# Kernel optimization log

Measured on AMD Instinct MI355X. Metric: run time of the kernel, lower is better.

The kernel has to match this reference:

```python
import math
import jax, jax.numpy as jnp
import numpy as np

N_HEADS = 8
EMB = 512
BATCH = 256
NKEYS = 2048
NEG_INF = -jnp.inf


def setup_inputs() -> dict:
    key = jax.random.key(0)
    kq, kk, kv, kw, km = jax.random.split(key, 5)
    query = jax.random.normal(kq, (BATCH, 1, EMB), dtype=jnp.float32)
    keys = jax.random.normal(kk, (BATCH, NKEYS, EMB), dtype=jnp.float32)
    value = jax.random.normal(kv, (BATCH, NKEYS, EMB), dtype=jnp.float32)
    W_o = jax.random.normal(kw, (EMB, EMB), dtype=jnp.float32) / math.sqrt(EMB)
    mask = jax.random.randint(km, (BATCH, 1, NKEYS), 0, 2) == 1  # bool [B,1,K]
    return {"query": query, "key": keys, "value": value, "W_o": W_o, "mask": mask}


def _make_heads(v):
    # [B, N, D] -> [H, B, N, D/H]
    b, n, d = v.shape
    return v.reshape(b, n, N_HEADS, d // N_HEADS).transpose(2, 0, 1, 3)


def reference(query, key, value, W_o, mask):
    qh = _make_heads(query)            # [H, B, 1, dh]
    kh = _make_heads(key)              # [H, B, K, dh]
    vh = _make_heads(value)            # [H, B, K, dh]
    dh = qh.shape[-1]
    # scaled dot-product scores: [H, B, 1, K]
    u = jnp.einsum("hbqd,hbkd->hbqk", qh, kh) / math.sqrt(dh)
    # boolean masking: mask [B,1,K] broadcasts over heads
    logits = jnp.where(mask[None], NEG_INF, u)
    a = jax.nn.softmax(logits, axis=-1)            # [H, B, 1, K]
    oh = jnp.einsum("hbqk,hbkd->hbqd", a, vh)      # [H, B, 1, dh]
    # unmake heads: [H,B,1,dh] -> [B,1,H*dh]
    b = oh.shape[1]
    merged = oh.transpose(1, 2, 0, 3).reshape(b, 1, N_HEADS * dh)
    out = merged @ W_o.T                           # Linear, no bias
    return out
```

## Files before the change

### kernel.cpp

```cpp
#include <hip/hip_runtime.h>


#define NB    256
#define NK    2048
#define EMBD  512
#define NH    8
#define DH    64
#define CHUNKS 8
#define CKEYS  256
#define PREC   520
#define ACP    520

__device__ __forceinline__ void barrier_lgkm() {
    asm volatile("s_waitcnt lgkmcnt(0)" ::: "memory");
    __builtin_amdgcn_s_barrier();
}

__device__ __forceinline__ float4 ld4(const float* p) {
    return *reinterpret_cast<const float4*>(p);
}

__global__ __launch_bounds__(256) void attn_chunk_kernel(
    const float* __restrict__ q,
    const float* __restrict__ kptr,
    const float* __restrict__ vptr,
    const int* __restrict__ mask,
    float* __restrict__ partials)
{
    const int bid  = blockIdx.x;
    const int b    = bid >> 3;
    const int c    = bid & 7;
    const int t    = threadIdx.x;
    const int w    = t >> 6;
    const int lane = t & 63;
    const int hq   = lane >> 3;
    const int sub  = lane & 7;

    __shared__ int   klist[CKEYS];
    __shared__ int   wavecnt[4];
    __shared__ float redl[4][NH];
    __shared__ float accb[4 * ACP];

    const float* qb = q + (size_t)b * EMBD + lane * 8;
    const float4 qa = ld4(qb);
    const float4 qc = ld4(qb + 4);
    const float* kb = kptr + (size_t)b * NK * EMBD + lane * 8;
    const float* vb = vptr + (size_t)b * NK * EMBD + lane * 8;
    const int*   mrow = mask + (size_t)b * NK + c * CKEYS;

    const int myk = w * 64 + lane;
    const int mk  = mrow[myk];
    const unsigned long long bal = __ballot(mk == 0);
    if (lane == 0) wavecnt[w] = __popcll(bal);
    __syncthreads();
    int off = 0, nun = 0;
    #pragma unroll
    for (int i = 0; i < 4; ++i) {
        const int cc = wavecnt[i];
        off += (i < w) ? cc : 0;
        nun += cc;
    }
    const unsigned long long below = (1ull << lane) - 1ull;
    if (!mk) klist[off + __popcll(bal & below)] = c * CKEYS + myk;
    __syncthreads();

    float lsum = 0.f;
    float4 a0 = {0.f, 0.f, 0.f, 0.f};
    float4 a1 = {0.f, 0.f, 0.f, 0.f};
    {
        int key0 = (w < nun) ? klist[w] : -1;
        int key1 = (w + 4 < nun) ? klist[w + 4] : -1;
        float4 ka = {0,0,0,0}, kc = {0,0,0,0};
        float4 va = {0,0,0,0}, vc = {0,0,0,0};
        if (key0 >= 0) {
            const float* kk = kb + (size_t)key0 * EMBD;
            const float* vv = vb + (size_t)key0 * EMBD;
            ka = ld4(kk); kc = ld4(kk + 4);
            va = ld4(vv); vc = ld4(vv + 4);
        }
        for (int slot = w; slot < nun; slot += 4) {
            float4 nka = {0,0,0,0}, nkc = {0,0,0,0};
            float4 nva = {0,0,0,0}, nvc = {0,0,0,0};
            if (key1 >= 0) {
                const float* kk = kb + (size_t)key1 * EMBD;
                const float* vv = vb + (size_t)key1 * EMBD;
                nka = ld4(kk); nkc = ld4(kk + 4);
                nva = ld4(vv); nvc = ld4(vv + 4);
            }
            const int key2 = (slot + 8 < nun) ? klist[slot + 8] : -1;
            float sv = qa.x * ka.x + qa.y * ka.y + qa.z * ka.z + qa.w * ka.w
                     + qc.x * kc.x + qc.y * kc.y + qc.z * kc.z + qc.w * kc.w;
            sv += __shfl_xor(sv, 1, 8);
            sv += __shfl_xor(sv, 2, 8);
            sv += __shfl_xor(sv, 4, 8);
            const float p = __expf(sv * 0.125f);
            lsum += p;
            a0.x = fmaf(p, va.x, a0.x); a0.y = fmaf(p, va.y, a0.y);
            a0.z = fmaf(p, va.z, a0.z); a0.w = fmaf(p, va.w, a0.w);
            a1.x = fmaf(p, vc.x, a1.x); a1.y = fmaf(p, vc.y, a1.y);
            a1.z = fmaf(p, vc.z, a1.z); a1.w = fmaf(p, vc.w, a1.w);
            key0 = key1; ka = nka; kc = nkc; va = nva; vc = nvc; key1 = key2;
        }
    }
    if (sub == 0) redl[w][hq] = lsum;
    *reinterpret_cast<float4*>(&accb[w * ACP + lane * 8])     = a0;
    *reinterpret_cast<float4*>(&accb[w * ACP + lane * 8 + 4]) = a1;
    __syncthreads();

    float* rec = partials + (size_t)bid * PREC;
    if (t < NH)
        rec[t] = redl[0][t] + redl[1][t] + redl[2][t] + redl[3][t];
    const float s0 = accb[t] + accb[ACP + t] + accb[2 * ACP + t] + accb[3 * ACP + t];
    const int t2 = t + 256;
    const float s1 = accb[t2] + accb[ACP + t2] + accb[2 * ACP + t2] + accb[3 * ACP + t2];
    rec[8 + t]  = s0;
    rec[8 + t2] = s1;
}

__global__ __launch_bounds__(256) void merge_proj_kernel(
    const float* __restrict__ partials,
    const float* __restrict__ Wo,
    float* __restrict__ out)
{
    const int bt = blockIdx.x >> 3;
    const int jt = blockIdx.x & 7;
    const int t  = threadIdx.x;
    __shared__ float mrow[8][EMBD];
    __shared__ float sden[64];

    if (t < 64) {
        const int bb = t >> 3, h = t & 7;
        const float* base = partials + (size_t)((bt * 8 + bb) * 8) * PREC;
        float d = 0.f;
        #pragma unroll
        for (int cc = 0; cc < 8; ++cc) d += base[cc * PREC + h];
        sden[t] = d;
    }
    #pragma unroll
    for (int e = 0; e < 16; ++e) {
        const int idx = e * 256 + t;
        const int bb = idx >> 9, el = idx & 511;
        const float* base = partials + (size_t)((bt * 8 + bb) * 8) * PREC + 8 + el;
        float s = 0.f;
        #pragma unroll
        for (int cc = 0; cc < 8; ++cc) s += base[cc * PREC];
        mrow[bb][el] = s;
    }
    __syncthreads();
    #pragma unroll
    for (int e = 0; e < 16; ++e) {
        const int idx = e * 256 + t;
        const int bb = idx >> 9, el = idx & 511;
        mrow[bb][el] /= sden[bb * 8 + (el >> 6)];
    }
    __syncthreads();

    const int j    = jt * 64 + (t & 63);
    const int brel = t >> 6;
    const float4* wrow = reinterpret_cast<const float4*>(Wo + (size_t)j * EMBD);
    const float4* m0 = reinterpret_cast<const float4*>(&mrow[brel][0]);
    const float4* m1 = reinterpret_cast<const float4*>(&mrow[brel + 4][0]);
    float s0 = 0.f, s1 = 0.f;
    #pragma unroll 4
    for (int i = 0; i < 128; ++i) {
        const float4 wv = wrow[i];
        const float4 x0 = m0[i];
        const float4 x1 = m1[i];
        s0 += wv.x * x0.x + wv.y * x0.y + wv.z * x0.z + wv.w * x0.w;
        s1 += wv.x * x1.x + wv.y * x1.y + wv.z * x1.z + wv.w * x1.w;
    }
    out[(size_t)(bt * 8 + brel) * EMBD + j] = s0;
    out[(size_t)(bt * 8 + brel + 4) * EMBD + j] = s1;
}

__global__ __launch_bounds__(1024) void attn_kernel(
    const float* __restrict__ q,
    const float* __restrict__ kptr,
    const float* __restrict__ vptr,
    const int* __restrict__ mask,
    float* __restrict__ merged)
{
    const int b    = blockIdx.x;
    const int t    = threadIdx.x;
    const int w    = t >> 6;
    const int lane = t & 63;
    const int hq   = lane >> 3;
    const int sub  = lane & 7;

    __shared__ int   klist[NK];
    __shared__ int   wavecnt[16];
    __shared__ float redl[16][NH];
    __shared__ float accb[16 * ACP];

    const float* qb = q + (size_t)b * EMBD + lane * 8;
    const float4 qa = ld4(qb);
    const float4 qc = ld4(qb + 4);
    const float* kb = kptr + (size_t)b * NK * EMBD + lane * 8;
    const float* vb = vptr + (size_t)b * NK * EMBD + lane * 8;
    const int*   mrow = mask + (size_t)b * NK;

    const int kA = w * 128 + lane;
    const int kB = kA + 64;
    const int mA = mrow[kA];
    const int mB = mrow[kB];
    const unsigned long long balA = __ballot(mA == 0);
    const unsigned long long balB = __ballot(mB == 0);
    if (lane == 0) wavecnt[w] = __popcll(balA) + __popcll(balB);
    barrier_lgkm();

    int off = 0, nun = 0;
    #pragma unroll
    for (int i = 0; i < 16; ++i) {
        const int c = wavecnt[i];
        off += (i < w) ? c : 0;
        nun += c;
    }
    const unsigned long long below = (1ull << lane) - 1ull;
    if (!mA) klist[off + __popcll(balA & below)] = kA;
    if (!mB) klist[off + __popcll(balA) + __popcll(balB & below)] = kB;
    barrier_lgkm();

    float lsum = 0.f;
    float4 a0 = {0.f, 0.f, 0.f, 0.f};
    float4 a1 = {0.f, 0.f, 0.f, 0.f};
    {
        int key0 = (w < nun) ? klist[w] : -1;
        int key1 = (w + 16 < nun) ? klist[w + 16] : -1;
        float4 ka = {0,0,0,0}, kc = {0,0,0,0};
        float4 va = {0,0,0,0}, vc = {0,0,0,0};
        if (key0 >= 0) {
            const float* kk = kb + (size_t)key0 * EMBD;
            const float* vv = vb + (size_t)key0 * EMBD;
            ka = ld4(kk); kc = ld4(kk + 4);
            va = ld4(vv); vc = ld4(vv + 4);
        }
        for (int slot = w; slot < nun; slot += 16) {
            float4 nka = {0,0,0,0}, nkc = {0,0,0,0};
            float4 nva = {0,0,0,0}, nvc = {0,0,0,0};
            if (key1 >= 0) {
                const float* kk = kb + (size_t)key1 * EMBD;
                const float* vv = vb + (size_t)key1 * EMBD;
                nka = ld4(kk); nkc = ld4(kk + 4);
                nva = ld4(vv); nvc = ld4(vv + 4);
            }
            const int key2 = (slot + 32 < nun) ? klist[slot + 32] : -1;
            float sv = qa.x * ka.x + qa.y * ka.y + qa.z * ka.z + qa.w * ka.w
                     + qc.x * kc.x + qc.y * kc.y + qc.z * kc.z + qc.w * kc.w;
            sv += __shfl_xor(sv, 1, 8);
            sv += __shfl_xor(sv, 2, 8);
            sv += __shfl_xor(sv, 4, 8);
            const float p = __expf(sv * 0.125f);
            lsum += p;
            a0.x = fmaf(p, va.x, a0.x); a0.y = fmaf(p, va.y, a0.y);
            a0.z = fmaf(p, va.z, a0.z); a0.w = fmaf(p, va.w, a0.w);
            a1.x = fmaf(p, vc.x, a1.x); a1.y = fmaf(p, vc.y, a1.y);
            a1.z = fmaf(p, vc.z, a1.z); a1.w = fmaf(p, vc.w, a1.w);
            key0 = key1; ka = nka; kc = nkc; va = nva; vc = nvc; key1 = key2;
        }
    }
    if (sub == 0) redl[w][hq] = lsum;
    *reinterpret_cast<float4*>(&accb[w * ACP + lane * 8])     = a0;
    *reinterpret_cast<float4*>(&accb[w * ACP + lane * 8 + 4]) = a1;
    barrier_lgkm();

    if (t < EMBD) {
        const int h = t >> 6;
        float den = 0.f;
        #pragma unroll
        for (int ww = 0; ww < 16; ++ww) den += redl[ww][h];
        float s = 0.f;
        #pragma unroll
        for (int ww = 0; ww < 16; ++ww) s += accb[ww * ACP + t];
        merged[(size_t)b * EMBD + t] = s / den;
    }
}

__global__ __launch_bounds__(256) void proj_kernel_inplace(
    const float* __restrict__ merged,
    const float* __restrict__ Wo,
    float* __restrict__ out)
{
    const int b = blockIdx.x;
    const int t = threadIdx.x;
    __shared__ float mrow[EMBD];
    *reinterpret_cast<float2*>(&mrow[t * 2]) =
        *reinterpret_cast<const float2*>(&merged[(size_t)b * EMBD + t * 2]);
    __syncthreads();

    const float4* mv = reinterpret_cast<const float4*>(mrow);
    #pragma unroll
    for (int half = 0; half < 2; ++half) {
        const int j = t + half * 256;
        const float4* wrow = reinterpret_cast<const float4*>(Wo + (size_t)j * EMBD);
        float s = 0.f;
        #pragma unroll 4
        for (int i = 0; i < EMBD / 4; ++i) {
            const float4 wv = wrow[i];
            const float4 qv = mv[i];
            s += wv.x * qv.x + wv.y * qv.y + wv.z * qv.z + wv.w * qv.w;
        }
        out[(size_t)b * EMBD + j] = s;
    }
}

extern "C" void kernel_launch(void* const* d_in, const int* in_sizes, int n_in,
                              void* d_out, int out_size, void* d_ws, size_t ws_size,
                              hipStream_t stream) {
    const float* q    = (const float*)d_in[0];
    const float* kptr = (const float*)d_in[1];
    const float* vptr = (const float*)d_in[2];
    const float* Wo   = (const float*)d_in[3];
    const int*   mask = (const int*)d_in[4];
    float* out = (float*)d_out;

    const size_t need = (size_t)NB * CHUNKS * PREC * sizeof(float);
    if (ws_size >= need) {
        float* partials = (float*)d_ws;
        attn_chunk_kernel<<<NB * CHUNKS, 256, 0, stream>>>(q, kptr, vptr, mask, partials);
        merge_proj_kernel<<<NB, 256, 0, stream>>>(partials, Wo, out);
    } else {
        attn_kernel<<<NB, 1024, 0, stream>>>(q, kptr, vptr, mask, out);
        proj_kernel_inplace<<<NB, 256, 0, stream>>>(out, Wo, out);
    }
}
```

Baseline: 228.9 us.

## Split attention into separate K-score and V-accumulate passes with LDS-staged probabilities

Each block now streams all unmasked keys first, computing exp scores into a shared-memory score table, then makes a second pass over the value rows weighted by those scores. Loads for K and V are no longer interleaved, so each phase streams one tensor with fewer live registers. Chunking also moves from 8 chunks of 256 keys per batch to 2 chunks of 1024 keys with 1024-thread blocks, which shrinks the partials buffer and the merge work. The cost is larger LDS use per block, an extra barrier between phases, and fewer, larger blocks.

```diff
diff --git a/kernel.cpp b/kernel.cpp
--- a/kernel.cpp
+++ b/kernel.cpp
@@ -6,10 +6,11 @@
 #define EMBD  512
 #define NH    8
 #define DH    64
-#define CHUNKS 8
-#define CKEYS  256
-#define PREC   520
-#define ACP    520
+#define CHUNKS 2
+#define CKEYS  1024
+#define SCP   2600
+#define ACP   520
+#define PREC  520
 
 __device__ __forceinline__ void barrier_lgkm() {
     asm volatile("s_waitcnt lgkmcnt(0)" ::: "memory");
@@ -20,7 +21,7 @@
     return *reinterpret_cast<const float4*>(p);
 }
 
-__global__ __launch_bounds__(256) void attn_chunk_kernel(
+__global__ __launch_bounds__(1024) void attn_chunk_kernel(
     const float* __restrict__ q,
     const float* __restrict__ kptr,
     const float* __restrict__ vptr,
@@ -28,93 +29,116 @@
     float* __restrict__ partials)
 {
     const int bid  = blockIdx.x;
-    const int b    = bid >> 3;
-    const int c    = bid & 7;
+    const int b    = bid >> 1;
+    const int c    = bid & 1;
     const int t    = threadIdx.x;
     const int w    = t >> 6;
     const int lane = t & 63;
     const int hq   = lane >> 3;
     const int sub  = lane & 7;
 
+    __shared__ float sc[NH][SCP];
     __shared__ int   klist[CKEYS];
-    __shared__ int   wavecnt[4];
-    __shared__ float redl[4][NH];
-    __shared__ float accb[4 * ACP];
+    __shared__ int   wavecnt[16];
+    __shared__ float redl[16][NH];
 
     const float* qb = q + (size_t)b * EMBD + lane * 8;
     const float4 qa = ld4(qb);
     const float4 qc = ld4(qb + 4);
     const float* kb = kptr + (size_t)b * NK * EMBD + lane * 8;
     const float* vb = vptr + (size_t)b * NK * EMBD + lane * 8;
-    const int*   mrow = mask + (size_t)b * NK + c * CKEYS;
-
-    const int myk = w * 64 + lane;
-    const int mk  = mrow[myk];
+    const int*   mrow = mask + (size_t)b * NK;
+
+    const int kG = c * CKEYS + w * 64 + lane;
+    const int mk = mrow[kG];
     const unsigned long long bal = __ballot(mk == 0);
     if (lane == 0) wavecnt[w] = __popcll(bal);
-    __syncthreads();
+    barrier_lgkm();
     int off = 0, nun = 0;
     #pragma unroll
-    for (int i = 0; i < 4; ++i) {
+    for (int i = 0; i < 16; ++i) {
         const int cc = wavecnt[i];
         off += (i < w) ? cc : 0;
         nun += cc;
     }
     const unsigned long long below = (1ull << lane) - 1ull;
-    if (!mk) klist[off + __popcll(bal & below)] = c * CKEYS + myk;
-    __syncthreads();
+    if (!mk) klist[off + __popcll(bal & below)] = kG;
+    barrier_lgkm();
 
     float lsum = 0.f;
-    float4 a0 = {0.f, 0.f, 0.f, 0.f};
-    float4 a1 = {0.f, 0.f, 0.f, 0.f};
     {
         int key0 = (w < nun) ? klist[w] : -1;
-        int key1 = (w + 4 < nun) ? klist[w + 4] : -1;
+        int key1 = (w + 16 < nun) ? klist[w + 16] : -1;
         float4 ka = {0,0,0,0}, kc = {0,0,0,0};
-        float4 va = {0,0,0,0}, vc = {0,0,0,0};
         if (key0 >= 0) {
             const float* kk = kb + (size_t)key0 * EMBD;
-            const float* vv = vb + (size_t)key0 * EMBD;
             ka = ld4(kk); kc = ld4(kk + 4);
-            va = ld4(vv); vc = ld4(vv + 4);
-        }
-        for (int slot = w; slot < nun; slot += 4) {
-            float4 nka = {0,0,0,0}, nkc = {0,0,0,0};
-            float4 nva = {0,0,0,0}, nvc = {0,0,0,0};
+        }
+        for (int slot = w; slot < nun; slot += 16) {
+            float4 na = {0,0,0,0}, nc = {0,0,0,0};
             if (key1 >= 0) {
                 const float* kk = kb + (size_t)key1 * EMBD;
-                const float* vv = vb + (size_t)key1 * EMBD;
-                nka = ld4(kk); nkc = ld4(kk + 4);
-                nva = ld4(vv); nvc = ld4(vv + 4);
+                na = ld4(kk); nc = ld4(kk + 4);
             }
-            const int key2 = (slot + 8 < nun) ? klist[slot + 8] : -1;
+            const int key2 = (slot + 32 < nun) ? klist[slot + 32] : -1;
             float sv = qa.x * ka.x + qa.y * ka.y + qa.z * ka.z + qa.w * ka.w
                      + qc.x * kc.x + qc.y * kc.y + qc.z * kc.z + qc.w * kc.w;
             sv += __shfl_xor(sv, 1, 8);
             sv += __shfl_xor(sv, 2, 8);
             sv += __shfl_xor(sv, 4, 8);
             const float p = __expf(sv * 0.125f);
+            if (sub == 0) sc[hq][key0] = p;
             lsum += p;
-            a0.x = fmaf(p, va.x, a0.x); a0.y = fmaf(p, va.y, a0.y);
-            a0.z = fmaf(p, va.z, a0.z); a0.w = fmaf(p, va.w, a0.w);
-            a1.x = fmaf(p, vc.x, a1.x); a1.y = fmaf(p, vc.y, a1.y);
-            a1.z = fmaf(p, vc.z, a1.z); a1.w = fmaf(p, vc.w, a1.w);
-            key0 = key1; ka = nka; kc = nkc; va = nva; vc = nvc; key1 = key2;
+            key0 = key1; ka = na; kc = nc; key1 = key2;
         }
     }
     if (sub == 0) redl[w][hq] = lsum;
+
+    int vk0 = (w < nun) ? klist[w] : -1;
+    int vk1 = (w + 16 < nun) ? klist[w + 16] : -1;
+    float4 va = {0,0,0,0}, vc = {0,0,0,0};
+    if (vk0 >= 0) {
+        const float* vv = vb + (size_t)vk0 * EMBD;
+        va = ld4(vv); vc = ld4(vv + 4);
+    }
+    barrier_lgkm();
+
+    float4 a0 = {0.f, 0.f, 0.f, 0.f};
+    float4 a1 = {0.f, 0.f, 0.f, 0.f};
+    for (int slot = w; slot < nun; slot += 16) {
+        float4 nva = {0,0,0,0}, nvc = {0,0,0,0};
+        if (vk1 >= 0) {
+            const float* vv = vb + (size_t)vk1 * EMBD;
+            nva = ld4(vv); nvc = ld4(vv + 4);
+        }
+        const int vk2 = (slot + 32 < nun) ? klist[slot + 32] : -1;
+        const float p = sc[hq][vk0];
+        a0.x = fmaf(p, va.x, a0.x); a0.y = fmaf(p, va.y, a0.y);
+        a0.z = fmaf(p, va.z, a0.z); a0.w = fmaf(p, va.w, a0.w);
+        a1.x = fmaf(p, vc.x, a1.x); a1.y = fmaf(p, vc.y, a1.y);
+        a1.z = fmaf(p, vc.z, a1.z); a1.w = fmaf(p, vc.w, a1.w);
+        vk0 = vk1; va = nva; vc = nvc; vk1 = vk2;
+    }
+
+    barrier_lgkm();
+    float* accb = &sc[0][0];
     *reinterpret_cast<float4*>(&accb[w * ACP + lane * 8])     = a0;
     *reinterpret_cast<float4*>(&accb[w * ACP + lane * 8 + 4]) = a1;
-    __syncthreads();
+    barrier_lgkm();
 
     float* rec = partials + (size_t)bid * PREC;
-    if (t < NH)
-        rec[t] = redl[0][t] + redl[1][t] + redl[2][t] + redl[3][t];
-    const float s0 = accb[t] + accb[ACP + t] + accb[2 * ACP + t] + accb[3 * ACP + t];
-    const int t2 = t + 256;
-    const float s1 = accb[t2] + accb[ACP + t2] + accb[2 * ACP + t2] + accb[3 * ACP + t2];
-    rec[8 + t]  = s0;
-    rec[8 + t2] = s1;
+    if (t < NH) {
+        float d = 0.f;
+        #pragma unroll
+        for (int ww = 0; ww < 16; ++ww) d += redl[ww][t];
+        rec[t] = d;
+    }
+    if (t < EMBD) {
+        float s = 0.f;
+        #pragma unroll
+        for (int ww = 0; ww < 16; ++ww) s += accb[ww * ACP + t];
+        rec[8 + t] = s;
+    }
 }
 
 __global__ __launch_bounds__(256) void merge_proj_kernel(
@@ -130,20 +154,20 @@
 
     if (t < 64) {
         const int bb = t >> 3, h = t & 7;
-        const float* base = partials + (size_t)((bt * 8 + bb) * 8) * PREC;
+        const float* base = partials + (size_t)((bt * 8 + bb) * CHUNKS) * PREC;
         float d = 0.f;
         #pragma unroll
-        for (int cc = 0; cc < 8; ++cc) d += base[cc * PREC + h];
+        for (int cc = 0; cc < CHUNKS; ++cc) d += base[cc * PREC + h];
         sden[t] = d;
     }
     #pragma unroll
     for (int e = 0; e < 16; ++e) {
         const int idx = e * 256 + t;
         const int bb = idx >> 9, el = idx & 511;
-        const float* base = partials + (size_t)((bt * 8 + bb) * 8) * PREC + 8 + el;
+        const float* base = partials + (size_t)((bt * 8 + bb) * CHUNKS) * PREC + 8 + el;
         float s = 0.f;
         #pragma unroll
-        for (int cc = 0; cc < 8; ++cc) s += base[cc * PREC];
+        for (int cc = 0; cc < CHUNKS; ++cc) s += base[cc * PREC];
         mrow[bb][el] = s;
     }
     __syncthreads();
@@ -187,10 +211,10 @@
     const int hq   = lane >> 3;
     const int sub  = lane & 7;
 
+    __shared__ float sc[NH][2052];
     __shared__ int   klist[NK];
     __shared__ int   wavecnt[16];
     __shared__ float redl[16][NH];
-    __shared__ float accb[16 * ACP];
 
     const float* qb = q + (size_t)b * EMBD + lane * 8;
     const float4 qa = ld4(qb);
@@ -211,9 +235,9 @@
     int off = 0, nun = 0;
     #pragma unroll
     for (int i = 0; i < 16; ++i) {
-        const int c = wavecnt[i];
-        off += (i < w) ? c : 0;
-        nun += c;
+        const int cv = wavecnt[i];
+        off += (i < w) ? cv : 0;
+        nun += cv;
     }
     const unsigned long long below = (1ull << lane) - 1ull;
     if (!mA) klist[off + __popcll(balA & below)] = kA;
@@ -221,27 +245,19 @@
     barrier_lgkm();
 
     float lsum = 0.f;
-    float4 a0 = {0.f, 0.f, 0.f, 0.f};
-    float4 a1 = {0.f, 0.f, 0.f, 0.f};
     {
         int key0 = (w < nun) ? klist[w] : -1;
         int key1 = (w + 16 < nun) ? klist[w + 16] : -1;
         float4 ka = {0,0,0,0}, kc = {0,0,0,0};
-        float4 va = {0,0,0,0}, vc = {0,0,0,0};
         if (key0 >= 0) {
             const float* kk = kb + (size_t)key0 * EMBD;
-            const float* vv = vb + (size_t)key0 * EMBD;
             ka = ld4(kk); kc = ld4(kk + 4);
-            va = ld4(vv); vc = ld4(vv + 4);
         }
         for (int slot = w; slot < nun; slot += 16) {
-            float4 nka = {0,0,0,0}, nkc = {0,0,0,0};
-            float4 nva = {0,0,0,0}, nvc = {0,0,0,0};
+            float4 na = {0,0,0,0}, nc = {0,0,0,0};
             if (key1 >= 0) {
                 const float* kk = kb + (size_t)key1 * EMBD;
-                const float* vv = vb + (size_t)key1 * EMBD;
-                nka = ld4(kk); nkc = ld4(kk + 4);
-                nva = ld4(vv); nvc = ld4(vv + 4);
+                na = ld4(kk); nc = ld4(kk + 4);
             }
             const int key2 = (slot + 32 < nun) ? klist[slot + 32] : -1;
             float sv = qa.x * ka.x + qa.y * ka.y + qa.z * ka.z + qa.w * ka.w
@@ -250,15 +266,41 @@
             sv += __shfl_xor(sv, 2, 8);
             sv += __shfl_xor(sv, 4, 8);
             const float p = __expf(sv * 0.125f);
+            if (sub == 0) sc[hq][key0] = p;
             lsum += p;
-            a0.x = fmaf(p, va.x, a0.x); a0.y = fmaf(p, va.y, a0.y);
-            a0.z = fmaf(p, va.z, a0.z); a0.w = fmaf(p, va.w, a0.w);
-            a1.x = fmaf(p, vc.x, a1.x); a1.y = fmaf(p, vc.y, a1.y);
-            a1.z = fmaf(p, vc.z, a1.z); a1.w = fmaf(p, vc.w, a1.w);
-            key0 = key1; ka = nka; kc = nkc; va = nva; vc = nvc; key1 = key2;
+            key0 = key1; ka = na; kc = nc; key1 = key2;
         }
     }
     if (sub == 0) redl[w][hq] = lsum;
+
+    int vk0 = (w < nun) ? klist[w] : -1;
+    int vk1 = (w + 16 < nun) ? klist[w + 16] : -1;
+    float4 va = {0,0,0,0}, vc = {0,0,0,0};
+    if (vk0 >= 0) {
+        const float* vv = vb + (size_t)vk0 * EMBD;
+        va = ld4(vv); vc = ld4(vv + 4);
+    }
+    barrier_lgkm();
+
+    float4 a0 = {0.f, 0.f, 0.f, 0.f};
+    float4 a1 = {0.f, 0.f, 0.f, 0.f};
+    for (int slot = w; slot < nun; slot += 16) {
+        float4 nva = {0,0,0,0}, nvc = {0,0,0,0};
+        if (vk1 >= 0) {
+            const float* vv = vb + (size_t)vk1 * EMBD;
+            nva = ld4(vv); nvc = ld4(vv + 4);
+        }
+        const int vk2 = (slot + 32 < nun) ? klist[slot + 32] : -1;
+        const float p = sc[hq][vk0];
+        a0.x = fmaf(p, va.x, a0.x); a0.y = fmaf(p, va.y, a0.y);
+        a0.z = fmaf(p, va.z, a0.z); a0.w = fmaf(p, va.w, a0.w);
+        a1.x = fmaf(p, vc.x, a1.x); a1.y = fmaf(p, vc.y, a1.y);
+        a1.z = fmaf(p, vc.z, a1.z); a1.w = fmaf(p, vc.w, a1.w);
+        vk0 = vk1; va = nva; vc = nvc; vk1 = vk2;
+    }
+
+    barrier_lgkm();
+    float* accb = &sc[0][0];
     *reinterpret_cast<float4*>(&accb[w * ACP + lane * 8])     = a0;
     *reinterpret_cast<float4*>(&accb[w * ACP + lane * 8 + 4]) = a1;
     barrier_lgkm();
@@ -316,7 +358,7 @@
     const size_t need = (size_t)NB * CHUNKS * PREC * sizeof(float);
     if (ws_size >= need) {
         float* partials = (float*)d_ws;
-        attn_chunk_kernel<<<NB * CHUNKS, 256, 0, stream>>>(q, kptr, vptr, mask, partials);
+        attn_chunk_kernel<<<NB * CHUNKS, 1024, 0, stream>>>(q, kptr, vptr, mask, partials);
         merge_proj_kernel<<<NB, 256, 0, stream>>>(partials, Wo, out);
     } else {
         attn_kernel<<<NB, 1024, 0, stream>>>(q, kptr, vptr, mask, out);
```

Result: faster. 207.8 us (-9.2%).
